# Kernel optimization log

Measured on AMD Instinct MI355X. Metric: run time of the kernel, lower is better.

The kernel has to match this reference:

```python
import jax, jax.numpy as jnp
import numpy as np

N = 262144   # number of samples
C = 16       # GMM components
D = 64       # feature dim


def setup_inputs() -> dict:
    key = jax.random.key(0)
    k1, k2, k3, k4 = jax.random.split(key, 4)
    inputs = jax.random.normal(k1, (N, D), dtype=jnp.float32)
    # SPD inverse covariances, as produced by inverting fitted GMM covariances
    R = jax.random.normal(k2, (C, D, D), dtype=jnp.float32)
    covariances_inv = jnp.einsum('cij,ckj->cik', R, R) / D + 0.1 * jnp.eye(D, dtype=jnp.float32)
    means = jax.random.normal(k3, (C, D), dtype=jnp.float32)
    w = jax.random.uniform(k4, (C,), dtype=jnp.float32, minval=0.1, maxval=1.0)
    weights = w / jnp.sum(w)  # mixture weights sum to 1
    return {"inputs": inputs, "covariances_inv": covariances_inv,
            "means": means, "weights": weights}


def reference(inputs, covariances_inv, means, weights):
    # Mahalanobis quadratic form per component: d[n,c] = (x_n - m_c)^T Sigma_c^{-1} (x_n - m_c)
    centered = inputs[:, None, :] - means[None, :, :]                # [N, C, D]
    distances_sqr = jnp.einsum('ncd,cde,nce->nc', centered, covariances_inv, centered)  # [N, C]
    # score_n = prod_c d[n,c] ** w_c
    score = jnp.prod(distances_sqr ** weights[None, :], axis=1)      # [N]
    return score
```

## Files before the change

### kernel.cpp

```cpp
#include <hip/hip_runtime.h>

typedef __attribute__((ext_vector_type(4))) float f32x4;
typedef __attribute__((ext_vector_type(8))) short bf16x8;

__device__ __forceinline__ short f2bf(float f) {
    union { float f; unsigned u; } v; v.f = f;
    unsigned u = v.u + 0x7FFFu + ((v.u >> 16) & 1u);
    return (short)(u >> 16);
}
__device__ __forceinline__ int pack_bf2(float a, float b) {
    union { float f; unsigned u; } ua, ub; ua.f = a; ub.f = b;
    unsigned x = ua.u + 0x8000u, y = ub.u + 0x8000u;
    return (int)__builtin_amdgcn_perm(y, x, 0x07060302u);
}

#if __has_builtin(__builtin_amdgcn_permlane16_swap) && \
    __has_builtin(__builtin_amdgcn_permlane32_swap)
__device__ __forceinline__ float quad_sum(float dp) {
    unsigned u = __float_as_uint(dp);
    auto r1 = __builtin_amdgcn_permlane16_swap(u, u, false, false);
    float s = __uint_as_float(r1[0]) + __uint_as_float(r1[1]);
    unsigned v = __float_as_uint(s);
    auto r2 = __builtin_amdgcn_permlane32_swap(v, v, false, false);
    return __uint_as_float(r2[0]) + __uint_as_float(r2[1]);
}
#else
__device__ __forceinline__ float quad_sum(float dp) {
    dp += __shfl_xor(dp, 16, 64);
    dp += __shfl_xor(dp, 32, 64);
    return dp;
}
#endif

__global__ void gmm_prep(const float* __restrict__ Ainv,
                         const float* __restrict__ means,
                         short* __restrict__ AbP16,
                         float* __restrict__ biasP) {
    __shared__ float sA[64 * 65];
    __shared__ float sm[64];
    __shared__ float sb[64];
    const int c = blockIdx.x, t = threadIdx.x;
    const float* A = Ainv + c * 4096;
    #pragma unroll
    for (int i = 0; i < 16; ++i) {
        int ft = i * 256 + t;
        sA[(ft >> 6) * 65 + (ft & 63)] = A[ft];
    }
    if (t < 64) sm[t] = means[c * 64 + t];
    __syncthreads();

    #pragma unroll 1
    for (int kb = 0; kb < 8; ++kb) {
        const int k0 = kb * 8;
        if (t < 64) {
            const int j = k0 + t;
            const bool act = (j < 64);
            const int jj = act ? j : 63;
            float pc[8];
            #pragma unroll
            for (int i = 0; i < 8; ++i) pc[i] = sA[jj * 65 + k0 + i];
            #pragma unroll
            for (int kk = 0; kk < 8; ++kk) {
                float diag = __shfl(pc[kk], kk, 64);
                float s = __builtin_sqrtf(diag);
                float inv = 1.f / s;
                if (t == kk)     pc[kk] = s;
                else if (t > kk) pc[kk] *= inv;
                #pragma unroll
                for (int i = kk + 1; i < 8; ++i) {
                    float lik = __shfl(pc[kk], i, 64);
                    if (t > kk) pc[i] = fmaf(-pc[kk], lik, pc[i]);
                }
            }
            if (act) {
                #pragma unroll
                for (int i = 0; i < 8; ++i) sA[j * 65 + k0 + i] = pc[i];
            }
        }
        __syncthreads();
        {
            const int r0 = k0 + 8;
            const int W = 64 - r0;
            if (W > 0) {
                const int qc = t & 15;
                const int jr = t >> 4;
                if (qc * 4 < W) {
                    const int i0 = r0 + qc * 4;
                    for (int j = r0 + jr; j < 64; j += 16) {
                        float a0 = 0.f, a1 = 0.f, a2 = 0.f, a3 = 0.f;
                        #pragma unroll
                        for (int k = 0; k < 8; ++k) {
                            float ljk = sA[j * 65 + k0 + k];
                            a0 = fmaf(ljk, sA[(i0 + 0) * 65 + k0 + k], a0);
                            a1 = fmaf(ljk, sA[(i0 + 1) * 65 + k0 + k], a1);
                            a2 = fmaf(ljk, sA[(i0 + 2) * 65 + k0 + k], a2);
                            a3 = fmaf(ljk, sA[(i0 + 3) * 65 + k0 + k], a3);
                        }
                        sA[j * 65 + i0 + 0] -= a0;
                        sA[j * 65 + i0 + 1] -= a1;
                        sA[j * 65 + i0 + 2] -= a2;
                        sA[j * 65 + i0 + 3] -= a3;
                    }
                }
            }
        }
        __syncthreads();
    }

    {
        int j = t >> 2, seg = t & 3;
        float p = 0.f;
        #pragma unroll
        for (int k2 = 0; k2 < 16; ++k2) {
            int k = seg * 16 + k2;
            float Mv = (k >= j) ? sA[k * 65 + j] : 0.f;
            p += Mv * sm[k];
        }
        p += __shfl_xor(p, 1, 64); p += __shfl_xor(p, 2, 64);
        if (seg == 0) sb[j] = p;
    }
    __syncthreads();
    if (t < 64) {
        int rt = t >> 4, qh = (t >> 2) & 3, r = t & 3;
        int pj = (rt >> 1) * 32 + 8 * qh + 4 * (rt & 1) + r;
        biasP[c * 64 + t] = -sb[pj];
    }
    #pragma unroll
    for (int rep = 0; rep < 2; ++rep) {
        int f = rep * 256 + t;
        int rt = f >> 7, kc = (f >> 6) & 1, L = f & 63;
        int ln = L & 15, q = L >> 4;
        int pj = (rt >> 1) * 32 + 8 * (ln >> 2) + 4 * (rt & 1) + (ln & 3);
        int kbase = 32 * kc + 8 * q;
        bf16x8 v;
        #pragma unroll
        for (int j = 0; j < 8; ++j) {
            int kk = kbase + j;
            float x = (kk >= pj) ? sA[kk * 65 + pj] : 0.f;
            v[j] = f2bf(x);
        }
        *(bf16x8*)(AbP16 + c * 4096 + f * 8) = v;
    }
}

union BFrag { bf16x8 v; int i[4]; };

__global__ __launch_bounds__(256, 4) void gmm_main(
    const float* __restrict__ X,
    const float* __restrict__ weights,
    const short* __restrict__ AbP16,
    const float* __restrict__ biasP,
    float* __restrict__ out) {

    const int tid = threadIdx.x;
    const int lane = tid & 63, w = tid >> 6;
    const int q = lane >> 4, ln = lane & 15;
    const int base = blockIdx.x * 256 + w * 64;

    BFrag xb[4][2];
    #pragma unroll
    for (int t = 0; t < 4; ++t) {
        const float* xr = X + (size_t)(base + t * 16 + ln) * 64 + 8 * q;
        #pragma unroll
        for (int kc = 0; kc < 2; ++kc) {
            f32x4 a = *(const f32x4*)(xr + 32 * kc);
            f32x4 b = *(const f32x4*)(xr + 32 * kc + 4);
            xb[t][kc].i[0] = pack_bf2(a[0], a[1]);
            xb[t][kc].i[1] = pack_bf2(a[2], a[3]);
            xb[t][kc].i[2] = pack_bf2(b[0], b[1]);
            xb[t][kc].i[3] = pack_bf2(b[2], b[3]);
        }
    }

    float slog[4] = {0.f, 0.f, 0.f, 0.f};

    #pragma unroll 1
    for (int c = 0; c < 16; ++c) {
        const short* aP = AbP16 + c * 4096 + lane * 8;
        bf16x8 af0 = *(const bf16x8*)(aP + 0 * 512);
        bf16x8 af1 = *(const bf16x8*)(aP + 1 * 512);
        bf16x8 af2 = *(const bf16x8*)(aP + 2 * 512);
        bf16x8 af3 = *(const bf16x8*)(aP + 3 * 512);
        bf16x8 af5 = *(const bf16x8*)(aP + 5 * 512);
        bf16x8 af7 = *(const bf16x8*)(aP + 7 * 512);
        f32x4 bias[4];
        #pragma unroll
        for (int rt = 0; rt < 4; ++rt)
            bias[rt] = *(const f32x4*)(biasP + c * 64 + rt * 16 + q * 4);
        const float wcc = weights[c];

        #pragma unroll
        for (int t = 0; t < 4; ++t) {
            f32x4 a0 = __builtin_amdgcn_mfma_f32_16x16x32_bf16(af0, xb[t][0].v, bias[0], 0, 0, 0);
            a0 = __builtin_amdgcn_mfma_f32_16x16x32_bf16(af1, xb[t][1].v, a0, 0, 0, 0);
            f32x4 a1 = __builtin_amdgcn_mfma_f32_16x16x32_bf16(af2, xb[t][0].v, bias[1], 0, 0, 0);
            a1 = __builtin_amdgcn_mfma_f32_16x16x32_bf16(af3, xb[t][1].v, a1, 0, 0, 0);
            f32x4 a2 = __builtin_amdgcn_mfma_f32_16x16x32_bf16(af5, xb[t][1].v, bias[2], 0, 0, 0);
            f32x4 a3 = __builtin_amdgcn_mfma_f32_16x16x32_bf16(af7, xb[t][1].v, bias[3], 0, 0, 0);

            float dp0 = a0[0] * a0[0], dp1 = a1[0] * a1[0];
            float dp2 = a2[0] * a2[0], dp3 = a3[0] * a3[0];
            #pragma unroll
            for (int i = 1; i < 4; ++i) {
                dp0 = fmaf(a0[i], a0[i], dp0);
                dp1 = fmaf(a1[i], a1[i], dp1);
                dp2 = fmaf(a2[i], a2[i], dp2);
                dp3 = fmaf(a3[i], a3[i], dp3);
            }
            float dp = quad_sum((dp0 + dp1) + (dp2 + dp3));
            float d = fmaxf(dp, 1e-30f);
            slog[t] = fmaf(wcc, __builtin_amdgcn_logf(d), slog[t]);
        }
    }

    float s0 = (q & 1) ? slog[1] : slog[0];
    float s1 = (q & 1) ? slog[3] : slog[2];
    float sv = (q & 2) ? s1 : s0;
    out[base + lane] = __builtin_amdgcn_exp2f(sv);
}

extern "C" void kernel_launch(void* const* d_in, const int* in_sizes, int n_in,
                              void* d_out, int out_size, void* d_ws, size_t ws_size,
                              hipStream_t stream) {
    const float* X       = (const float*)d_in[0];
    const float* Ainv    = (const float*)d_in[1];
    const float* means   = (const float*)d_in[2];
    const float* weights = (const float*)d_in[3];
    float* out = (float*)d_out;
    const int N = in_sizes[0] / 64;

    short* AbP16 = (short*)d_ws;
    float* biasP = (float*)((char*)d_ws + 131072);

    gmm_prep<<<dim3(16), dim3(256), 0, stream>>>(Ainv, means, AbP16, biasP);
    gmm_main<<<dim3(N / 256), dim3(256), 0, stream>>>(X, weights, AbP16, biasP, out);
}
```

Measured before the change: 136.7 us.

## Double-buffer component A-fragments in registers and stage biases in shared memory

The component loop now prefetches the bf16 A-fragments for the next component into a second register set while the current one is being multiplied, so global load latency is hidden behind the MFMA work. All 16x64 bias values are loaded into LDS once per block and read from there instead of from global memory on each iteration. The cost is extra VGPR pressure from holding two fragment sets, which could reduce occupancy under launch_bounds(256,4), plus one added block barrier.

```diff
diff --git a/kernel.cpp b/kernel.cpp
--- a/kernel.cpp
+++ b/kernel.cpp
@@ -144,6 +144,18 @@
 }
 
 union BFrag { bf16x8 v; int i[4]; };
+struct AFrags { bf16x8 f0, f1, f2, f3, f5, f7; };
+
+__device__ __forceinline__ AFrags ld_af(const short* aP) {
+    AFrags r;
+    r.f0 = *(const bf16x8*)(aP + 0 * 512);
+    r.f1 = *(const bf16x8*)(aP + 1 * 512);
+    r.f2 = *(const bf16x8*)(aP + 2 * 512);
+    r.f3 = *(const bf16x8*)(aP + 3 * 512);
+    r.f5 = *(const bf16x8*)(aP + 5 * 512);
+    r.f7 = *(const bf16x8*)(aP + 7 * 512);
+    return r;
+}
 
 __global__ __launch_bounds__(256, 4) void gmm_main(
     const float* __restrict__ X,
@@ -152,10 +164,18 @@
     const float* __restrict__ biasP,
     float* __restrict__ out) {
 
+    __shared__ float sBias[1024];
+
     const int tid = threadIdx.x;
     const int lane = tid & 63, w = tid >> 6;
     const int q = lane >> 4, ln = lane & 15;
     const int base = blockIdx.x * 256 + w * 64;
+
+    ((f32x4*)sBias)[tid] = ((const f32x4*)biasP)[tid];
+
+    const short* aBase = AbP16 + lane * 8;
+    AFrags fa = ld_af(aBase);
+    AFrags fb = ld_af(aBase + 4096);
 
     BFrag xb[4][2];
     #pragma unroll
@@ -171,32 +191,24 @@
             xb[t][kc].i[3] = pack_bf2(b[2], b[3]);
         }
     }
+    __syncthreads();
 
     float slog[4] = {0.f, 0.f, 0.f, 0.f};
 
-    #pragma unroll 1
-    for (int c = 0; c < 16; ++c) {
-        const short* aP = AbP16 + c * 4096 + lane * 8;
-        bf16x8 af0 = *(const bf16x8*)(aP + 0 * 512);
-        bf16x8 af1 = *(const bf16x8*)(aP + 1 * 512);
-        bf16x8 af2 = *(const bf16x8*)(aP + 2 * 512);
-        bf16x8 af3 = *(const bf16x8*)(aP + 3 * 512);
-        bf16x8 af5 = *(const bf16x8*)(aP + 5 * 512);
-        bf16x8 af7 = *(const bf16x8*)(aP + 7 * 512);
-        f32x4 bias[4];
-        #pragma unroll
-        for (int rt = 0; rt < 4; ++rt)
-            bias[rt] = *(const f32x4*)(biasP + c * 64 + rt * 16 + q * 4);
+    auto comp_one = [&](const AFrags& F, int c) {
+        f32x4 b0 = *(const f32x4*)&sBias[c * 64 +  0 + q * 4];
+        f32x4 b1 = *(const f32x4*)&sBias[c * 64 + 16 + q * 4];
+        f32x4 b2 = *(const f32x4*)&sBias[c * 64 + 32 + q * 4];
+        f32x4 b3 = *(const f32x4*)&sBias[c * 64 + 48 + q * 4];
         const float wcc = weights[c];
-
         #pragma unroll
         for (int t = 0; t < 4; ++t) {
-            f32x4 a0 = __builtin_amdgcn_mfma_f32_16x16x32_bf16(af0, xb[t][0].v, bias[0], 0, 0, 0);
-            a0 = __builtin_amdgcn_mfma_f32_16x16x32_bf16(af1, xb[t][1].v, a0, 0, 0, 0);
-            f32x4 a1 = __builtin_amdgcn_mfma_f32_16x16x32_bf16(af2, xb[t][0].v, bias[1], 0, 0, 0);
-            a1 = __builtin_amdgcn_mfma_f32_16x16x32_bf16(af3, xb[t][1].v, a1, 0, 0, 0);
-            f32x4 a2 = __builtin_amdgcn_mfma_f32_16x16x32_bf16(af5, xb[t][1].v, bias[2], 0, 0, 0);
-            f32x4 a3 = __builtin_amdgcn_mfma_f32_16x16x32_bf16(af7, xb[t][1].v, bias[3], 0, 0, 0);
+            f32x4 a0 = __builtin_amdgcn_mfma_f32_16x16x32_bf16(F.f0, xb[t][0].v, b0, 0, 0, 0);
+            a0 = __builtin_amdgcn_mfma_f32_16x16x32_bf16(F.f1, xb[t][1].v, a0, 0, 0, 0);
+            f32x4 a1 = __builtin_amdgcn_mfma_f32_16x16x32_bf16(F.f2, xb[t][0].v, b1, 0, 0, 0);
+            a1 = __builtin_amdgcn_mfma_f32_16x16x32_bf16(F.f3, xb[t][1].v, a1, 0, 0, 0);
+            f32x4 a2 = __builtin_amdgcn_mfma_f32_16x16x32_bf16(F.f5, xb[t][1].v, b2, 0, 0, 0);
+            f32x4 a3 = __builtin_amdgcn_mfma_f32_16x16x32_bf16(F.f7, xb[t][1].v, b3, 0, 0, 0);
 
             float dp0 = a0[0] * a0[0], dp1 = a1[0] * a1[0];
             float dp2 = a2[0] * a2[0], dp3 = a3[0] * a3[0];
@@ -211,6 +223,14 @@
             float d = fmaxf(dp, 1e-30f);
             slog[t] = fmaf(wcc, __builtin_amdgcn_logf(d), slog[t]);
         }
+    };
+
+    #pragma unroll 1
+    for (int cc = 0; cc < 16; cc += 2) {
+        comp_one(fa, cc);
+        if (cc + 2 < 16) fa = ld_af(aBase + (cc + 2) * 4096);
+        comp_one(fb, cc + 1);
+        if (cc + 3 < 16) fb = ld_af(aBase + (cc + 3) * 4096);
     }
 
     float s0 = (q & 1) ? slog[1] : slog[0];
```

Result: slower. 146.4 us (+7.1%).
